# Optimization experiments

Hardware: AMD Instinct MI355X
Metric: run time of the kernel (lower is better)

Reference implementation:

```python
import jax, jax.numpy as jnp
import numpy as np

FRAME_SIZE = 160
LPC_N = 16
T = 2400  # pcm_chunk_size = 160 * 15
B = 1024

SCALE = 255.0 / 32768.0
SCALE_1 = 32768.0 / 255.0
LOG256 = float(np.log(256.0))


def u2l(u):
    # mu-law (0..255) -> linear
    u = u - 128.0
    s = jnp.sign(u)
    u = jnp.abs(u)
    return s * SCALE_1 * (jnp.exp(u / 128.0 * LOG256) - 1.0)


def l2u(x):
    # linear -> mu-law (0..255)
    s = jnp.sign(x)
    x = jnp.abs(x)
    u = s * (128.0 * jnp.log1p(SCALE * x) / LOG256)
    return jnp.clip(128.0 + u, 0.0, 255.0)


def setup_inputs() -> dict:
    key = jax.random.key(0)
    k1, k2 = jax.random.split(key)
    sig = jax.random.uniform(k1, (B, T, 1), dtype=jnp.float32) * 255.0
    lpc = jax.random.normal(k2, (B, 15, LPC_N), dtype=jnp.float32) * 0.1
    return {"sig": sig, "lpc": lpc}


def reference(sig, lpc):
    # decode mu-law input to linear domain
    xt = u2l(sig)[:, :, 0]                          # (B, T)
    # zero-pad LPC_N samples at the front (history)
    xp = jnp.pad(xt, ((0, 0), (LPC_N, 0)))           # (B, T + LPC_N)
    # 16 shifted views: tap i sees xp[:, LPC_N - i : LPC_N - i + T]
    cX = jnp.stack([xp[:, LPC_N - i:LPC_N - i + T] for i in range(LPC_N)],
                   axis=2)                           # (B, T, LPC_N)
    # repeat per-frame LPC coeffs over the 160 samples of each frame
    lpc_rep = jnp.repeat(lpc, FRAME_SIZE, axis=1)    # (B, T, LPC_N)
    pred = -jnp.sum(lpc_rep * cX, axis=2, keepdims=True)  # (B, T, 1)
    return l2u(pred)
```

## Files before the change

kernel.cpp:

```cpp
#include <hip/hip_runtime.h>
#include <hip/hip_bf16.h>

#define T_LEN 2400
#define LPC_N 16
#define FRAME 160
#define CHUNK 800
#define NGRP  (CHUNK / 4)
#define BLOCK 256

__global__ __launch_bounds__(BLOCK)
void diff_pred_26319559589961_kernel(const float* __restrict__ sig,
                                     const float* __restrict__ lpc,
                                     float* __restrict__ out)
{
    __shared__ float xs[CHUNK + LPC_N];

    const int b   = blockIdx.y;
    const int t0  = blockIdx.x * CHUNK;
    const int tid = threadIdx.x;

    if (tid < (CHUNK + LPC_N) / 4) {
        const int t_in = t0 - LPC_N + 4 * tid;
        float4 r;
        if (t_in >= 0) {
            const float4 v = *(const float4*)(sig + (size_t)b * T_LEN + t_in);
            const float ux = v.x - 128.0f, uy = v.y - 128.0f,
                        uz = v.z - 128.0f, uw = v.w - 128.0f;
            r.x = copysignf((32768.0f/255.0f) * (exp2f(fabsf(ux) * 0.0625f) - 1.0f), ux);
            r.y = copysignf((32768.0f/255.0f) * (exp2f(fabsf(uy) * 0.0625f) - 1.0f), uy);
            r.z = copysignf((32768.0f/255.0f) * (exp2f(fabsf(uz) * 0.0625f) - 1.0f), uz);
            r.w = copysignf((32768.0f/255.0f) * (exp2f(fabsf(uw) * 0.0625f) - 1.0f), uw);
        } else {
            r = make_float4(0.0f, 0.0f, 0.0f, 0.0f);
        }
        *(float4*)(xs + 4 * tid) = r;
    }
    __syncthreads();

    if (tid < NGRP) {
        const int t     = t0 + 4 * tid;
        const int frame = t / FRAME;
        const float4* c = (const float4*)(lpc + ((size_t)b * 15 + frame) * LPC_N);
        const float4 c0 = c[0], c1 = c[1], c2 = c[2], c3 = c[3];

        float r[20];
        *(float4*)(r +  0) = *(const float4*)(xs + 4 * tid +  0);
        *(float4*)(r +  4) = *(const float4*)(xs + 4 * tid +  4);
        *(float4*)(r +  8) = *(const float4*)(xs + 4 * tid +  8);
        *(float4*)(r + 12) = *(const float4*)(xs + 4 * tid + 12);
        *(float4*)(r + 16) = *(const float4*)(xs + 4 * tid + 16);

        const float cf[16] = { c0.x, c0.y, c0.z, c0.w,
                               c1.x, c1.y, c1.z, c1.w,
                               c2.x, c2.y, c2.z, c2.w,
                               c3.x, c3.y, c3.z, c3.w };

        float4 o;
        float* op = &o.x;
        #pragma unroll
        for (int k = 0; k < 4; ++k) {
            float acc = 0.0f;
            #pragma unroll
            for (int i = 0; i < LPC_N; ++i)
                acc += cf[i] * r[16 + k - i];
            const float pred = -acc;
            const float u = copysignf(
                16.0f * __log2f(1.0f + (255.0f/32768.0f) * fabsf(pred)), pred);
            op[k] = fminf(fmaxf(128.0f + u, 0.0f), 255.0f);
        }
        *(float4*)(out + (size_t)b * T_LEN + t) = o;
    }
}

extern "C" void kernel_launch(void* const* d_in, const int* in_sizes, int n_in,
                              void* d_out, int out_size, void* d_ws, size_t ws_size,
                              hipStream_t stream) {
    const float* sig = (const float*)d_in[0];
    const float* lpc = (const float*)d_in[1];
    float* out = (float*)d_out;

    const int B = in_sizes[0] / T_LEN;
    dim3 grid(T_LEN / CHUNK, B);
    diff_pred_26319559589961_kernel<<<grid, BLOCK, 0, stream>>>(sig, lpc, out);
}
```

Before: 65.10 us.

## Drop shared-memory staging; each thread loads and decodes its own history window

Removes the LDS buffer and __syncthreads, so each thread loads 20 input samples directly from global memory and recomputes the mu-law decode for them. The grid is flattened to a 1D launch with every thread active, replacing the old layout where 56 of 256 threads idled in the compute phase. The cost is 5x redundant global loads (served mostly from cache) and 5x redundant exp2 work per sample. Padding is now applied by loading 128.0, which decodes to zero, so the output is unchanged.

```diff
diff --git a/kernel.cpp b/kernel.cpp
--- a/kernel.cpp
+++ b/kernel.cpp
@@ -4,72 +4,56 @@
 #define T_LEN 2400
 #define LPC_N 16
 #define FRAME 160
-#define CHUNK 800
-#define NGRP  (CHUNK / 4)
 #define BLOCK 256
+#define GROUPS_PER_ROW (T_LEN / 4)
 
 __global__ __launch_bounds__(BLOCK)
 void diff_pred_26319559589961_kernel(const float* __restrict__ sig,
                                      const float* __restrict__ lpc,
                                      float* __restrict__ out)
 {
-    __shared__ float xs[CHUNK + LPC_N];
+    const int g = blockIdx.x * BLOCK + threadIdx.x;
+    const int b = g / GROUPS_PER_ROW;
+    const int t = (g - b * GROUPS_PER_ROW) * 4;
 
-    const int b   = blockIdx.y;
-    const int t0  = blockIdx.x * CHUNK;
-    const int tid = threadIdx.x;
+    const float* sp = sig + (size_t)b * T_LEN + (t - LPC_N);
+    float r[20];
+    #pragma unroll
+    for (int j = 0; j < 5; ++j) {
+        const int start = t - LPC_N + 4 * j;
+        float4 v = make_float4(128.0f, 128.0f, 128.0f, 128.0f);
+        if (start >= 0)
+            v = *(const float4*)(sp + 4 * j);
+        const float ux = v.x - 128.0f, uy = v.y - 128.0f,
+                    uz = v.z - 128.0f, uw = v.w - 128.0f;
+        r[4*j + 0] = copysignf((32768.0f/255.0f) * (exp2f(fabsf(ux) * 0.0625f) - 1.0f), ux);
+        r[4*j + 1] = copysignf((32768.0f/255.0f) * (exp2f(fabsf(uy) * 0.0625f) - 1.0f), uy);
+        r[4*j + 2] = copysignf((32768.0f/255.0f) * (exp2f(fabsf(uz) * 0.0625f) - 1.0f), uz);
+        r[4*j + 3] = copysignf((32768.0f/255.0f) * (exp2f(fabsf(uw) * 0.0625f) - 1.0f), uw);
+    }
 
-    if (tid < (CHUNK + LPC_N) / 4) {
-        const int t_in = t0 - LPC_N + 4 * tid;
-        float4 r;
-        if (t_in >= 0) {
-            const float4 v = *(const float4*)(sig + (size_t)b * T_LEN + t_in);
-            const float ux = v.x - 128.0f, uy = v.y - 128.0f,
-                        uz = v.z - 128.0f, uw = v.w - 128.0f;
-            r.x = copysignf((32768.0f/255.0f) * (exp2f(fabsf(ux) * 0.0625f) - 1.0f), ux);
-            r.y = copysignf((32768.0f/255.0f) * (exp2f(fabsf(uy) * 0.0625f) - 1.0f), uy);
-            r.z = copysignf((32768.0f/255.0f) * (exp2f(fabsf(uz) * 0.0625f) - 1.0f), uz);
-            r.w = copysignf((32768.0f/255.0f) * (exp2f(fabsf(uw) * 0.0625f) - 1.0f), uw);
-        } else {
-            r = make_float4(0.0f, 0.0f, 0.0f, 0.0f);
-        }
-        *(float4*)(xs + 4 * tid) = r;
+    const int frame = t / FRAME;
+    const float4* c = (const float4*)(lpc + ((size_t)b * 15 + frame) * LPC_N);
+    const float4 c0 = c[0], c1 = c[1], c2 = c[2], c3 = c[3];
+    const float cf[16] = { c0.x, c0.y, c0.z, c0.w,
+                           c1.x, c1.y, c1.z, c1.w,
+                           c2.x, c2.y, c2.z, c2.w,
+                           c3.x, c3.y, c3.z, c3.w };
+
+    float4 o;
+    float* op = &o.x;
+    #pragma unroll
+    for (int k = 0; k < 4; ++k) {
+        float acc = 0.0f;
+        #pragma unroll
+        for (int i = 0; i < LPC_N; ++i)
+            acc += cf[i] * r[16 + k - i];
+        const float pred = -acc;
+        const float u = copysignf(
+            16.0f * __log2f(1.0f + (255.0f/32768.0f) * fabsf(pred)), pred);
+        op[k] = fminf(fmaxf(128.0f + u, 0.0f), 255.0f);
     }
-    __syncthreads();
-
-    if (tid < NGRP) {
-        const int t     = t0 + 4 * tid;
-        const int frame = t / FRAME;
-        const float4* c = (const float4*)(lpc + ((size_t)b * 15 + frame) * LPC_N);
-        const float4 c0 = c[0], c1 = c[1], c2 = c[2], c3 = c[3];
-
-        float r[20];
-        *(float4*)(r +  0) = *(const float4*)(xs + 4 * tid +  0);
-        *(float4*)(r +  4) = *(const float4*)(xs + 4 * tid +  4);
-        *(float4*)(r +  8) = *(const float4*)(xs + 4 * tid +  8);
-        *(float4*)(r + 12) = *(const float4*)(xs + 4 * tid + 12);
-        *(float4*)(r + 16) = *(const float4*)(xs + 4 * tid + 16);
-
-        const float cf[16] = { c0.x, c0.y, c0.z, c0.w,
-                               c1.x, c1.y, c1.z, c1.w,
-                               c2.x, c2.y, c2.z, c2.w,
-                               c3.x, c3.y, c3.z, c3.w };
-
-        float4 o;
-        float* op = &o.x;
-        #pragma unroll
-        for (int k = 0; k < 4; ++k) {
-            float acc = 0.0f;
-            #pragma unroll
-            for (int i = 0; i < LPC_N; ++i)
-                acc += cf[i] * r[16 + k - i];
-            const float pred = -acc;
-            const float u = copysignf(
-                16.0f * __log2f(1.0f + (255.0f/32768.0f) * fabsf(pred)), pred);
-            op[k] = fminf(fmaxf(128.0f + u, 0.0f), 255.0f);
-        }
-        *(float4*)(out + (size_t)b * T_LEN + t) = o;
-    }
+    *(float4*)(out + (size_t)b * T_LEN + t) = o;
 }
 
 extern "C" void kernel_launch(void* const* d_in, const int* in_sizes, int n_in,
@@ -80,6 +64,6 @@
     float* out = (float*)d_out;
 
     const int B = in_sizes[0] / T_LEN;
-    dim3 grid(T_LEN / CHUNK, B);
-    diff_pred_26319559589961_kernel<<<grid, BLOCK, 0, stream>>>(sig, lpc, out);
+    const int total_groups = B * GROUPS_PER_ROW;
+    diff_pred_26319559589961_kernel<<<total_groups / BLOCK, BLOCK, 0, stream>>>(sig, lpc, out);
 }
```

Measured after the change: 69.66 us. 1.07x slower.
